# Performance work log

Measured on AMD Instinct MI355X. Metric: run time of the kernel, lower is better.

The kernel has to match this reference:

```python
import jax, jax.numpy as jnp
import numpy as np

NEG_SLOPE = 0.2
EPS = 1e-16  # PyG softmax denominator epsilon


def add_self_loops(edge_index, num_nodes):
    loop = jnp.arange(num_nodes, dtype=edge_index.dtype)
    src = jnp.concatenate([edge_index[0], loop])
    dst = jnp.concatenate([edge_index[1], loop])
    return src, dst


def gat_conv(x, src, dst, W, att_src, att_dst, bias, num_nodes):
    H, C = att_src.shape
    h = (x @ W).reshape(num_nodes, H, C)            # [N,H,C]
    a_s = jnp.einsum('nhc,hc->nh', h, att_src)      # [N,H]
    a_d = jnp.einsum('nhc,hc->nh', h, att_dst)
    e = jax.nn.leaky_relu(a_s[src] + a_d[dst], NEG_SLOPE)  # [E,H]
    m = jax.ops.segment_max(e, dst, num_segments=num_nodes)
    e = jnp.exp(e - m[dst])
    s = jax.ops.segment_sum(e, dst, num_segments=num_nodes)
    alpha = e / (s[dst] + EPS)                      # [E,H]
    out = jax.ops.segment_sum(h[src] * alpha[:, :, None], dst,
                              num_segments=num_nodes)  # [N,H,C]
    return out.reshape(num_nodes, H * C) + bias


def setup_inputs() -> dict:
    key = jax.random.key(0)
    ks = jax.random.split(key, 10)
    N, E, F, Ch = 50000, 800000, 128, 64
    sc = lambda f: 1.0 / np.sqrt(f)
    return {
        'x': jax.random.normal(ks[0], (N, F), jnp.float32),
        'edge_index': jax.random.randint(ks[1], (2, E), 0, N, jnp.int64),
        'W1': jax.random.normal(ks[2], (F, 4 * Ch), jnp.float32) * sc(F),
        'att_src1': jax.random.normal(ks[3], (4, Ch), jnp.float32) * sc(Ch),
        'att_dst1': jax.random.normal(ks[4], (4, Ch), jnp.float32) * sc(Ch),
        'b1': jnp.zeros((4 * Ch,), jnp.float32),
        'W2': jax.random.normal(ks[5], (4 * Ch, Ch), jnp.float32) * sc(4 * Ch),
        'att_src2': jax.random.normal(ks[6], (1, Ch), jnp.float32) * sc(Ch),
        'att_dst2': jax.random.normal(ks[7], (1, Ch), jnp.float32) * sc(Ch),
        'b2': jnp.zeros((Ch,), jnp.float32),
    }


def reference(x, edge_index, W1, att_src1, att_dst1, b1, W2, att_src2, att_dst2, b2):
    N = x.shape[0]
    src, dst = add_self_loops(edge_index, N)
    # dropout layers are inference no-ops
    h = gat_conv(x, src, dst, W1, att_src1, att_dst1, b1, N)
    h = jax.nn.elu(h)
    out = gat_conv(h, src, dst, W2, att_src2, att_dst2, b2, N)
    return out
```

## Files before the change

### kernel.cpp

```cpp
#include <hip/hip_runtime.h>
#include <hip/hip_bf16.h>
#include <stdint.h>


typedef __attribute__((ext_vector_type(8))) short bf16x8;
typedef __attribute__((ext_vector_type(4))) float f32x4;

__device__ __forceinline__ float bf2f(__hip_bfloat16 v) { return __bfloat162float(v); }
__device__ __forceinline__ float bfbits2f(unsigned short s) {
  union { uint32_t u; float f; } v; v.u = ((uint32_t)s) << 16; return v.f;
}
__device__ __forceinline__ unsigned short f2bfbits(float f) {
  union { float f; uint32_t u; } v; v.f = f;
  uint32_t u = v.u;
  return (unsigned short)((u + 0x7fffu + ((u >> 16) & 1u)) >> 16);
}

template <bool BF>
__device__ __forceinline__ float loadF(const void* p, size_t i) {
  if (BF) return bf2f(((const __hip_bfloat16*)p)[i]);
  return ((const float*)p)[i];
}
template <bool I64>
__device__ __forceinline__ int loadI(const void* p, size_t i) {
  if (I64) return (int)((const long long*)p)[i];
  return ((const int*)p)[i];
}
__device__ __forceinline__ float lrelu(float v) { return fmaxf(v, 0.2f * v); }

__global__ __launch_bounds__(256) void detect_zero(
    const uint32_t* __restrict__ xbits, const uint32_t* __restrict__ eibits,
    int* __restrict__ flags, int* __restrict__ zero_region, int nzero) {
  if (blockIdx.x == 0) {
    if (threadIdx.x < 64) {
      const int l = threadIdx.x;
      uint32_t u = xbits[l];
      uint32_t e = (u >> 23) & 0xffu;
      bool plausible = (e < 160u && e > 90u) || (u & 0x7fffffffu) == 0u;
      unsigned long long m1 = __ballot(plausible);
      bool z = (eibits[2 * l + 1] == 0u);
      unsigned long long m2 = __ballot(z);
      if (l == 0) {
        flags[0] = (__popcll(m1) < 32) ? 1 : 0;
        flags[1] = (m2 == ~0ULL) ? 1 : 0;
      }
    }
    return;
  }
  int i = (blockIdx.x - 1) * 256 + threadIdx.x;
  if (i < nzero) zero_region[i] = 0;
}

__global__ __launch_bounds__(256) void prep_all(
    const void* __restrict__ x, unsigned short* __restrict__ xb, size_t nx,
    const void* __restrict__ W1, unsigned short* __restrict__ w1t, int K1, int N1,
    const void* __restrict__ W2, unsigned short* __restrict__ w2t, int K2, int N2,
    int nb_cast, int nb_t1, const int* __restrict__ flags) {
  const int b = blockIdx.x;
  const bool f = flags[0] != 0;
  if (b < nb_cast) {
    size_t i = ((size_t)b * 256 + threadIdx.x) * 4;
    if (i >= nx) return;
    ushort4 o;
    if (f) {
      o = *(const ushort4*)((const unsigned short*)x + i);
    } else {
      float4 v = *(const float4*)((const float*)x + i);
      o.x = f2bfbits(v.x); o.y = f2bfbits(v.y);
      o.z = f2bfbits(v.z); o.w = f2bfbits(v.w);
    }
    *(ushort4*)(xb + i) = o;
  } else if (b < nb_cast + nb_t1) {
    int idx = (b - nb_cast) * 256 + threadIdx.x;
    if (idx >= K1 * N1) return;
    int k = idx / N1, n = idx - k * N1;
    float v = f ? loadF<true>(W1, idx) : loadF<false>(W1, idx);
    w1t[(size_t)n * K1 + k] = f2bfbits(v);
  } else {
    int idx = (b - nb_cast - nb_t1) * 256 + threadIdx.x;
    if (idx >= K2 * N2) return;
    int k = idx / N2, n = idx - k * N2;
    float v = f ? loadF<true>(W2, idx) : loadF<false>(W2, idx);
    w2t[(size_t)n * K2 + k] = f2bfbits(v);
  }
}

template <int KC, int NT, int HB>
__global__ __launch_bounds__(256, 4) void gemm_mfma_att(
    const unsigned short* __restrict__ A,
    const unsigned short* __restrict__ BT,
    unsigned short* __restrict__ C,
    const void* __restrict__ att_s, const void* __restrict__ att_d,
    float* __restrict__ as_o, float* __restrict__ ad_o,
    float* __restrict__ wself_o,
    int M, int Htot, const int* __restrict__ flags) {
  const int lane = threadIdx.x & 63;
  const int col = lane & 15;
  const int quad = lane >> 4;
  const int m0 = blockIdx.x * 64 + (threadIdx.x >> 6) * 16;
  const int n0 = blockIdx.y * (NT * 16);
  const int NCOL = Htot * 64;

  int gm = m0 + col;
  if (gm > M - 1) gm = M - 1;
  const unsigned short* arow = A + (size_t)gm * KC + quad * 8;
  const unsigned short* bbase = BT + (size_t)(n0 + col) * KC + quad * 8;

  f32x4 acc[NT] = {};
#pragma unroll
  for (int k0 = 0; k0 < KC; k0 += 32) {
    bf16x8 a = *(const bf16x8*)(arow + k0);
#pragma unroll
    for (int s = 0; s < NT; s++) {
      bf16x8 b = *(const bf16x8*)(bbase + (size_t)s * 16 * KC + k0);
      acc[s] = __builtin_amdgcn_mfma_f32_16x16x32_bf16(a, b, acc[s], 0, 0, 0);
    }
  }
#pragma unroll
  for (int s = 0; s < NT; s++)
#pragma unroll
    for (int r = 0; r < 4; r++) {
      int m = m0 + quad * 4 + r;
      if (m < M) C[(size_t)m * NCOL + n0 + s * 16 + col] = f2bfbits(acc[s][r]);
    }
  const int SC = NT / HB;
  const bool f = flags[0] != 0;
#pragma unroll
  for (int h = 0; h < HB; h++) {
    const int gh = blockIdx.y * HB + h;
    float ps[4] = {0.f, 0.f, 0.f, 0.f};
    float pd[4] = {0.f, 0.f, 0.f, 0.f};
#pragma unroll
    for (int j = 0; j < SC; j++) {
      int s = h * SC + j;
      int ci = gh * 64 + j * 16 + col;
      float av = f ? loadF<true>(att_s, ci) : loadF<false>(att_s, ci);
      float dv = f ? loadF<true>(att_d, ci) : loadF<false>(att_d, ci);
#pragma unroll
      for (int r = 0; r < 4; r++) {
        ps[r] += acc[s][r] * av;
        pd[r] += acc[s][r] * dv;
      }
    }
#pragma unroll
    for (int o = 1; o < 16; o <<= 1) {
#pragma unroll
      for (int r = 0; r < 4; r++) {
        ps[r] += __shfl_xor(ps[r], o);
        pd[r] += __shfl_xor(pd[r], o);
      }
    }
    if (col == 0) {
#pragma unroll
      for (int r = 0; r < 4; r++) {
        int m = m0 + quad * 4 + r;
        if (m < M) {
          as_o[m * Htot + gh] = ps[r];
          ad_o[m * Htot + gh] = pd[r];
          wself_o[m * Htot + gh] = __expf(lrelu(ps[r] + pd[r]));
        }
      }
    }
  }
}

__global__ void hist_kernel(const void* __restrict__ ei, int E,
                            int* __restrict__ deg, const int* __restrict__ flags) {
  int e = blockIdx.x * blockDim.x + threadIdx.x;
  if (e >= E) return;
  int d = flags[1] ? loadI<true>(ei, (size_t)E + e) : loadI<false>(ei, (size_t)E + e);
  atomicAdd(&deg[d], 1);
}

__global__ __launch_bounds__(256) void scan_block_sums(const int* __restrict__ deg,
                                                       int* __restrict__ bsum, int n) {
  __shared__ int buf[256];
  const int t = threadIdx.x;
  const int i = blockIdx.x * 256 + t;
  buf[t] = (i < n) ? deg[i] : 0;
  __syncthreads();
  for (int o = 128; o > 0; o >>= 1) {
    if (t < o) buf[t] += buf[t + o];
    __syncthreads();
  }
  if (t == 0) bsum[blockIdx.x] = buf[0];
}

__global__ __launch_bounds__(256) void scan_bsums(int* __restrict__ bsum, int nb) {
  __shared__ int buf[256];
  const int t = threadIdx.x;
  int orig = (t < nb) ? bsum[t] : 0;
  buf[t] = orig;
  __syncthreads();
  for (int o = 1; o < 256; o <<= 1) {
    int v = (t >= o) ? buf[t - o] : 0;
    __syncthreads();
    buf[t] += v;
    __syncthreads();
  }
  if (t < nb) bsum[t] = buf[t] - orig;
}

__global__ __launch_bounds__(256) void scan_finalize(const int* __restrict__ deg,
                                                     const int* __restrict__ bsum,
                                                     int* __restrict__ row_start, int n) {
  __shared__ int buf[256];
  const int t = threadIdx.x;
  const int i = blockIdx.x * 256 + t;
  int v = (i < n) ? deg[i] : 0;
  buf[t] = v;
  __syncthreads();
  for (int o = 1; o < 256; o <<= 1) {
    int x = (t >= o) ? buf[t - o] : 0;
    __syncthreads();
    buf[t] += x;
    __syncthreads();
  }
  if (i < n) row_start[i + 1] = bsum[blockIdx.x] + buf[t];
  if (i == 0) row_start[0] = 0;
}

__global__ void scatter_edges(const void* __restrict__ ei, int E,
                              const int* __restrict__ row_start,
                              int* __restrict__ cursor, int* __restrict__ col_src,
                              const int* __restrict__ flags) {
  int e = blockIdx.x * blockDim.x + threadIdx.x;
  if (e >= E) return;
  int s, d;
  if (flags[1]) { s = loadI<true>(ei, e);  d = loadI<true>(ei, (size_t)E + e); }
  else          { s = loadI<false>(ei, e); d = loadI<false>(ei, (size_t)E + e); }
  int pos = atomicAdd(&cursor[d], 1);
  col_src[row_start[d] + pos] = s;
}

__global__ __launch_bounds__(256) void aggregate4(
    const unsigned short* __restrict__ h_in,
    const float* __restrict__ wselfA,
    const float* __restrict__ as_,
    const float* __restrict__ ad_,
    const int* __restrict__ row_start, const int* __restrict__ col_src,
    const void* __restrict__ bias,
    unsigned short* __restrict__ out,
    int N, const int* __restrict__ flags) {
  const int dst = blockIdx.x * 4 + (threadIdx.x >> 6);
  if (dst >= N) return;
  const int l = threadIdx.x & 63;
  const int h = l >> 4;
  const int rs = row_start[dst];
  const int dg = row_start[dst + 1] - rs;
  const float ws = wselfA[dst * 4 + h];
  const float adv = ad_[dst * 4 + h];

  float a0, a1, a2, a3;
  {
    ushort4 sv = *(const ushort4*)(h_in + (size_t)dst * 256 + 4 * l);
    a0 = ws * bfbits2f(sv.x);
    a1 = ws * bfbits2f(sv.y);
    a2 = ws * bfbits2f(sv.z);
    a3 = ws * bfbits2f(sv.w);
  }
  float p = 0.f;
#pragma unroll 4
  for (int i = 0; i < dg; i++) {
    int sn = col_src[rs + i];
    float w = __expf(lrelu(as_[(size_t)sn * 4 + h] + adv));
    p += w;
    ushort4 sv = *(const ushort4*)(h_in + (size_t)sn * 256 + 4 * l);
    a0 += w * bfbits2f(sv.x);
    a1 += w * bfbits2f(sv.y);
    a2 += w * bfbits2f(sv.z);
    a3 += w * bfbits2f(sv.w);
  }
  const float inv = 1.0f / (p + ws + 1e-16f);
  const bool f = flags[0] != 0;
  float b0, b1, b2, b3;
  if (f) {
    b0 = loadF<true>(bias, 4 * l + 0); b1 = loadF<true>(bias, 4 * l + 1);
    b2 = loadF<true>(bias, 4 * l + 2); b3 = loadF<true>(bias, 4 * l + 3);
  } else {
    b0 = loadF<false>(bias, 4 * l + 0); b1 = loadF<false>(bias, 4 * l + 1);
    b2 = loadF<false>(bias, 4 * l + 2); b3 = loadF<false>(bias, 4 * l + 3);
  }
  float o0 = a0 * inv + b0, o1 = a1 * inv + b1;
  float o2 = a2 * inv + b2, o3 = a3 * inv + b3;
  o0 = o0 > 0.f ? o0 : __expf(o0) - 1.f;
  o1 = o1 > 0.f ? o1 : __expf(o1) - 1.f;
  o2 = o2 > 0.f ? o2 : __expf(o2) - 1.f;
  o3 = o3 > 0.f ? o3 : __expf(o3) - 1.f;
  ushort4 ov;
  ov.x = f2bfbits(o0); ov.y = f2bfbits(o1); ov.z = f2bfbits(o2); ov.w = f2bfbits(o3);
  *(ushort4*)(out + (size_t)dst * 256 + 4 * l) = ov;
}

__global__ __launch_bounds__(256) void aggregate1(
    const unsigned short* __restrict__ h_in,
    const float* __restrict__ wselfA,
    const float* __restrict__ as_,
    const float* __restrict__ ad_,
    const int* __restrict__ row_start, const int* __restrict__ col_src,
    const void* __restrict__ bias,
    void* __restrict__ out, int N, const int* __restrict__ flags) {
  const int dst = blockIdx.x * 4 + (threadIdx.x >> 6);
  if (dst >= N) return;
  const int l = threadIdx.x & 63;
  const int el = l & 15;
  const int slot = l >> 4;
  const int rs = row_start[dst];
  const int dg = row_start[dst + 1] - rs;
  const float ws = wselfA[dst];
  const float adv = ad_[dst];

  float a0 = 0.f, a1 = 0.f, a2 = 0.f, a3 = 0.f, p = 0.f;
  if (slot == 0) {
    ushort4 sv = *(const ushort4*)(h_in + (size_t)dst * 64 + 4 * el);
    a0 = ws * bfbits2f(sv.x);
    a1 = ws * bfbits2f(sv.y);
    a2 = ws * bfbits2f(sv.z);
    a3 = ws * bfbits2f(sv.w);
  }
#pragma unroll 2
  for (int i = slot; i < dg; i += 4) {
    int sn = col_src[rs + i];
    float w = __expf(lrelu(as_[sn] + adv));
    p += w;
    ushort4 sv = *(const ushort4*)(h_in + (size_t)sn * 64 + 4 * el);
    a0 += w * bfbits2f(sv.x);
    a1 += w * bfbits2f(sv.y);
    a2 += w * bfbits2f(sv.z);
    a3 += w * bfbits2f(sv.w);
  }
  a0 += __shfl_xor(a0, 16); a0 += __shfl_xor(a0, 32);
  a1 += __shfl_xor(a1, 16); a1 += __shfl_xor(a1, 32);
  a2 += __shfl_xor(a2, 16); a2 += __shfl_xor(a2, 32);
  a3 += __shfl_xor(a3, 16); a3 += __shfl_xor(a3, 32);
  p  += __shfl_xor(p, 16);  p  += __shfl_xor(p, 32);

  if (slot == 0) {
    const float inv = 1.0f / (p + ws + 1e-16f);
    const bool f = flags[0] != 0;
    float b0, b1, b2, b3;
    if (f) {
      b0 = loadF<true>(bias, 4 * el + 0); b1 = loadF<true>(bias, 4 * el + 1);
      b2 = loadF<true>(bias, 4 * el + 2); b3 = loadF<true>(bias, 4 * el + 3);
    } else {
      b0 = loadF<false>(bias, 4 * el + 0); b1 = loadF<false>(bias, 4 * el + 1);
      b2 = loadF<false>(bias, 4 * el + 2); b3 = loadF<false>(bias, 4 * el + 3);
    }
    float o0 = a0 * inv + b0, o1 = a1 * inv + b1;
    float o2 = a2 * inv + b2, o3 = a3 * inv + b3;
    size_t ob = (size_t)dst * 64 + 4 * el;
    if (f) {
      ushort4 ov;
      ov.x = f2bfbits(o0); ov.y = f2bfbits(o1);
      ov.z = f2bfbits(o2); ov.w = f2bfbits(o3);
      *(ushort4*)((unsigned short*)out + ob) = ov;
    } else {
      float4 ov; ov.x = o0; ov.y = o1; ov.z = o2; ov.w = o3;
      *(float4*)((float*)out + ob) = ov;
    }
  }
}

extern "C" void kernel_launch(void* const* d_in, const int* in_sizes, int n_in,
                              void* d_out, int out_size, void* d_ws, size_t ws_size,
                              hipStream_t stream) {
  const void* x    = d_in[0];
  const void* ei   = d_in[1];
  const void* W1   = d_in[2];
  const void* as1w = d_in[3];
  const void* ad1w = d_in[4];
  const void* b1   = d_in[5];
  const void* W2   = d_in[6];
  const void* as2w = d_in[7];
  const void* ad2w = d_in[8];
  const void* b2   = d_in[9];

  const int N  = out_size / 64;
  const int F  = in_sizes[0] / N;
  const int E  = in_sizes[1] / 2;
  const int H1 = in_sizes[3] / 64;
  const int D1 = H1 * 64;
  const int D2 = 64;

  size_t off = 0;
  auto alloc = [&](size_t bytes) -> void* {
    void* p = (char*)d_ws + off;
    off += (bytes + 255) & ~(size_t)255;
    return p;
  };
  int* flags = (int*)alloc(2 * sizeof(int));
  __hip_bfloat16* h1 = (__hip_bfloat16*)alloc((size_t)N * D1 * 2);
  __hip_bfloat16* x2 = (__hip_bfloat16*)alloc((size_t)N * D1 * 2);
  __hip_bfloat16* h2 = h1;
  unsigned short* xb  = (unsigned short*)alloc((size_t)N * F * 2);
  unsigned short* w1t = (unsigned short*)alloc((size_t)D1 * F * 2);
  unsigned short* w2t = (unsigned short*)alloc((size_t)D2 * D1 * 2);
  float* as1 = (float*)alloc((size_t)N * H1 * 4);
  float* ad1 = (float*)alloc((size_t)N * H1 * 4);
  float* wself1 = (float*)alloc((size_t)N * H1 * 4);
  float* as2 = (float*)alloc((size_t)N * 4);
  float* ad2 = (float*)alloc((size_t)N * 4);
  float* wself2 = (float*)alloc((size_t)N * 4);
  int* zero_region = (int*)alloc((size_t)2 * N * 4);
  int* deg = zero_region;
  int* cursor = zero_region + N;
  int* row_start = (int*)alloc((size_t)(N + 1) * 4);
  int* col_src = (int*)alloc((size_t)E * 4);
  int* bsum = (int*)alloc((size_t)256 * 4);
  (void)ws_size; (void)n_in;

  const int nb = (N + 255) / 256;
  const int eb = (E + 255) / 256;
  const int db = (N + 3) / 4;
  const int gb = (N + 63) / 64;
  const int nzero = 2 * N;
  const int zb = (nzero + 255) / 256;

  detect_zero<<<1 + zb, 256, 0, stream>>>((const uint32_t*)x, (const uint32_t*)ei,
                                          flags, zero_region, nzero);
  hist_kernel<<<eb, 256, 0, stream>>>(ei, E, deg, flags);
  scan_block_sums<<<nb, 256, 0, stream>>>(deg, bsum, N);
  scan_bsums<<<1, 256, 0, stream>>>(bsum, nb);
  scan_finalize<<<nb, 256, 0, stream>>>(deg, bsum, row_start, N);
  scatter_edges<<<eb, 256, 0, stream>>>(ei, E, row_start, cursor, col_src, flags);

  const size_t nx = (size_t)N * F;
  const int nb_cast = (int)((nx / 4 + 255) / 256);
  const int nb_t1 = (F * D1 + 255) / 256;
  const int nb_t2 = (D1 * D2 + 255) / 256;
  prep_all<<<nb_cast + nb_t1 + nb_t2, 256, 0, stream>>>(
      x, xb, nx, W1, w1t, F, D1, W2, w2t, D1, D2, nb_cast, nb_t1, flags);

  gemm_mfma_att<128, 8, 2><<<dim3(gb, 2), 256, 0, stream>>>(
      xb, w1t, (unsigned short*)h1, as1w, ad1w, as1, ad1, wself1, N, H1, flags);
  aggregate4<<<db, 256, 0, stream>>>((const unsigned short*)h1, wself1, as1, ad1,
                                     row_start, col_src, b1,
                                     (unsigned short*)x2, N, flags);

  gemm_mfma_att<256, 4, 1><<<dim3(gb, 1), 256, 0, stream>>>(
      (const unsigned short*)x2, w2t, (unsigned short*)h2, as2w, ad2w,
      as2, ad2, wself2, N, 1, flags);
  aggregate1<<<db, 256, 0, stream>>>((const unsigned short*)h2, wself2, as2, ad2,
                                     row_start, col_src, b2, d_out, N, flags);
}
```

Measured before the change: 331.3 us.

## Merge CSR build into fewer launches: fuse hist with prep, one-pass scan, scatter with GEMM1

```diff
diff --git a/kernel.cpp b/kernel.cpp
--- a/kernel.cpp
+++ b/kernel.cpp
@@ -51,33 +51,36 @@
   if (i < nzero) zero_region[i] = 0;
 }
 
-__global__ __launch_bounds__(256) void prep_all(
+__global__ __launch_bounds__(256) void hist_prep(
+    const void* __restrict__ ei, int E, int* __restrict__ deg,
     const void* __restrict__ x, unsigned short* __restrict__ xb, size_t nx,
     const void* __restrict__ W1, unsigned short* __restrict__ w1t, int K1, int N1,
     const void* __restrict__ W2, unsigned short* __restrict__ w2t, int K2, int N2,
-    int nb_cast, int nb_t1, const int* __restrict__ flags) {
+    int eb, int nb_cast, int nb_t1, const int* __restrict__ flags) {
   const int b = blockIdx.x;
   const bool f = flags[0] != 0;
-  if (b < nb_cast) {
-    size_t i = ((size_t)b * 256 + threadIdx.x) * 4;
+  if (b < eb) {
+    int e = b * 256 + threadIdx.x;
+    if (e >= E) return;
+    int d = flags[1] ? loadI<true>(ei, (size_t)E + e) : loadI<false>(ei, (size_t)E + e);
+    atomicAdd(&deg[d], 1);
+  } else if (b < eb + nb_cast) {
+    if (f) return;
+    size_t i = ((size_t)(b - eb) * 256 + threadIdx.x) * 4;
     if (i >= nx) return;
+    float4 v = *(const float4*)((const float*)x + i);
     ushort4 o;
-    if (f) {
-      o = *(const ushort4*)((const unsigned short*)x + i);
-    } else {
-      float4 v = *(const float4*)((const float*)x + i);
-      o.x = f2bfbits(v.x); o.y = f2bfbits(v.y);
-      o.z = f2bfbits(v.z); o.w = f2bfbits(v.w);
-    }
+    o.x = f2bfbits(v.x); o.y = f2bfbits(v.y);
+    o.z = f2bfbits(v.z); o.w = f2bfbits(v.w);
     *(ushort4*)(xb + i) = o;
-  } else if (b < nb_cast + nb_t1) {
-    int idx = (b - nb_cast) * 256 + threadIdx.x;
+  } else if (b < eb + nb_cast + nb_t1) {
+    int idx = (b - eb - nb_cast) * 256 + threadIdx.x;
     if (idx >= K1 * N1) return;
     int k = idx / N1, n = idx - k * N1;
     float v = f ? loadF<true>(W1, idx) : loadF<false>(W1, idx);
     w1t[(size_t)n * K1 + k] = f2bfbits(v);
   } else {
-    int idx = (b - nb_cast - nb_t1) * 256 + threadIdx.x;
+    int idx = (b - eb - nb_cast - nb_t1) * 256 + threadIdx.x;
     if (idx >= K2 * N2) return;
     int k = idx / N2, n = idx - k * N2;
     float v = f ? loadF<true>(W2, idx) : loadF<false>(W2, idx);
@@ -85,126 +88,11 @@
   }
 }
 
-template <int KC, int NT, int HB>
-__global__ __launch_bounds__(256, 4) void gemm_mfma_att(
-    const unsigned short* __restrict__ A,
-    const unsigned short* __restrict__ BT,
-    unsigned short* __restrict__ C,
-    const void* __restrict__ att_s, const void* __restrict__ att_d,
-    float* __restrict__ as_o, float* __restrict__ ad_o,
-    float* __restrict__ wself_o,
-    int M, int Htot, const int* __restrict__ flags) {
-  const int lane = threadIdx.x & 63;
-  const int col = lane & 15;
-  const int quad = lane >> 4;
-  const int m0 = blockIdx.x * 64 + (threadIdx.x >> 6) * 16;
-  const int n0 = blockIdx.y * (NT * 16);
-  const int NCOL = Htot * 64;
-
-  int gm = m0 + col;
-  if (gm > M - 1) gm = M - 1;
-  const unsigned short* arow = A + (size_t)gm * KC + quad * 8;
-  const unsigned short* bbase = BT + (size_t)(n0 + col) * KC + quad * 8;
-
-  f32x4 acc[NT] = {};
-#pragma unroll
-  for (int k0 = 0; k0 < KC; k0 += 32) {
-    bf16x8 a = *(const bf16x8*)(arow + k0);
-#pragma unroll
-    for (int s = 0; s < NT; s++) {
-      bf16x8 b = *(const bf16x8*)(bbase + (size_t)s * 16 * KC + k0);
-      acc[s] = __builtin_amdgcn_mfma_f32_16x16x32_bf16(a, b, acc[s], 0, 0, 0);
-    }
-  }
-#pragma unroll
-  for (int s = 0; s < NT; s++)
-#pragma unroll
-    for (int r = 0; r < 4; r++) {
-      int m = m0 + quad * 4 + r;
-      if (m < M) C[(size_t)m * NCOL + n0 + s * 16 + col] = f2bfbits(acc[s][r]);
-    }
-  const int SC = NT / HB;
-  const bool f = flags[0] != 0;
-#pragma unroll
-  for (int h = 0; h < HB; h++) {
-    const int gh = blockIdx.y * HB + h;
-    float ps[4] = {0.f, 0.f, 0.f, 0.f};
-    float pd[4] = {0.f, 0.f, 0.f, 0.f};
-#pragma unroll
-    for (int j = 0; j < SC; j++) {
-      int s = h * SC + j;
-      int ci = gh * 64 + j * 16 + col;
-      float av = f ? loadF<true>(att_s, ci) : loadF<false>(att_s, ci);
-      float dv = f ? loadF<true>(att_d, ci) : loadF<false>(att_d, ci);
-#pragma unroll
-      for (int r = 0; r < 4; r++) {
-        ps[r] += acc[s][r] * av;
-        pd[r] += acc[s][r] * dv;
-      }
-    }
-#pragma unroll
-    for (int o = 1; o < 16; o <<= 1) {
-#pragma unroll
-      for (int r = 0; r < 4; r++) {
-        ps[r] += __shfl_xor(ps[r], o);
-        pd[r] += __shfl_xor(pd[r], o);
-      }
-    }
-    if (col == 0) {
-#pragma unroll
-      for (int r = 0; r < 4; r++) {
-        int m = m0 + quad * 4 + r;
-        if (m < M) {
-          as_o[m * Htot + gh] = ps[r];
-          ad_o[m * Htot + gh] = pd[r];
-          wself_o[m * Htot + gh] = __expf(lrelu(ps[r] + pd[r]));
-        }
-      }
-    }
-  }
-}
-
-__global__ void hist_kernel(const void* __restrict__ ei, int E,
-                            int* __restrict__ deg, const int* __restrict__ flags) {
-  int e = blockIdx.x * blockDim.x + threadIdx.x;
-  if (e >= E) return;
-  int d = flags[1] ? loadI<true>(ei, (size_t)E + e) : loadI<false>(ei, (size_t)E + e);
-  atomicAdd(&deg[d], 1);
-}
-
-__global__ __launch_bounds__(256) void scan_block_sums(const int* __restrict__ deg,
-                                                       int* __restrict__ bsum, int n) {
+__global__ __launch_bounds__(256) void scan_onepass(
+    const int* __restrict__ deg, int* __restrict__ row_start,
+    int* __restrict__ total, int n) {
   __shared__ int buf[256];
-  const int t = threadIdx.x;
-  const int i = blockIdx.x * 256 + t;
-  buf[t] = (i < n) ? deg[i] : 0;
-  __syncthreads();
-  for (int o = 128; o > 0; o >>= 1) {
-    if (t < o) buf[t] += buf[t + o];
-    __syncthreads();
-  }
-  if (t == 0) bsum[blockIdx.x] = buf[0];
-}
-
-__global__ __launch_bounds__(256) void scan_bsums(int* __restrict__ bsum, int nb) {
-  __shared__ int buf[256];
-  const int t = threadIdx.x;
-  int orig = (t < nb) ? bsum[t] : 0;
-  buf[t] = orig;
-  __syncthreads();
-  for (int o = 1; o < 256; o <<= 1) {
-    int v = (t >= o) ? buf[t - o] : 0;
-    __syncthreads();
-    buf[t] += v;
-    __syncthreads();
-  }
-  if (t < nb) bsum[t] = buf[t] - orig;
-}
-
-__global__ __launch_bounds__(256) void scan_finalize(const int* __restrict__ deg,
-                                                     const int* __restrict__ bsum,
-                                                     int* __restrict__ row_start, int n) {
-  __shared__ int buf[256];
+  __shared__ int sbase;
   const int t = threadIdx.x;
   const int i = blockIdx.x * 256 + t;
   int v = (i < n) ? deg[i] : 0;
@@ -216,21 +104,131 @@
     buf[t] += x;
     __syncthreads();
   }
-  if (i < n) row_start[i + 1] = bsum[blockIdx.x] + buf[t];
-  if (i == 0) row_start[0] = 0;
-}
-
-__global__ void scatter_edges(const void* __restrict__ ei, int E,
-                              const int* __restrict__ row_start,
-                              int* __restrict__ cursor, int* __restrict__ col_src,
-                              const int* __restrict__ flags) {
-  int e = blockIdx.x * blockDim.x + threadIdx.x;
-  if (e >= E) return;
-  int s, d;
-  if (flags[1]) { s = loadI<true>(ei, e);  d = loadI<true>(ei, (size_t)E + e); }
-  else          { s = loadI<false>(ei, e); d = loadI<false>(ei, (size_t)E + e); }
-  int pos = atomicAdd(&cursor[d], 1);
-  col_src[row_start[d] + pos] = s;
+  if (t == 255) sbase = atomicAdd(total, buf[255]);
+  __syncthreads();
+  if (i < n) row_start[i] = sbase + buf[t] - v;
+}
+
+template <int KC, int NT, int HB>
+__device__ __forceinline__ void gemm_body(
+    int bx, int by, int tid,
+    const unsigned short* __restrict__ A,
+    const unsigned short* __restrict__ BT,
+    unsigned short* __restrict__ C,
+    const void* __restrict__ att_s, const void* __restrict__ att_d,
+    float* __restrict__ as_o, float* __restrict__ ad_o,
+    float* __restrict__ wself_o,
+    int M, int Htot, bool f) {
+  const int lane = tid & 63;
+  const int col = lane & 15;
+  const int quad = lane >> 4;
+  const int m0 = bx * 64 + (tid >> 6) * 16;
+  const int n0 = by * (NT * 16);
+  const int NCOL = Htot * 64;
+
+  int gm = m0 + col;
+  if (gm > M - 1) gm = M - 1;
+  const unsigned short* arow = A + (size_t)gm * KC + quad * 8;
+  const unsigned short* bbase = BT + (size_t)(n0 + col) * KC + quad * 8;
+
+  f32x4 acc[NT] = {};
+#pragma unroll
+  for (int k0 = 0; k0 < KC; k0 += 32) {
+    bf16x8 a = *(const bf16x8*)(arow + k0);
+#pragma unroll
+    for (int s = 0; s < NT; s++) {
+      bf16x8 b = *(const bf16x8*)(bbase + (size_t)s * 16 * KC + k0);
+      acc[s] = __builtin_amdgcn_mfma_f32_16x16x32_bf16(a, b, acc[s], 0, 0, 0);
+    }
+  }
+#pragma unroll
+  for (int s = 0; s < NT; s++)
+#pragma unroll
+    for (int r = 0; r < 4; r++) {
+      int m = m0 + quad * 4 + r;
+      if (m < M) C[(size_t)m * NCOL + n0 + s * 16 + col] = f2bfbits(acc[s][r]);
+    }
+  const int SC = NT / HB;
+#pragma unroll
+  for (int h = 0; h < HB; h++) {
+    const int gh = by * HB + h;
+    float ps[4] = {0.f, 0.f, 0.f, 0.f};
+    float pd[4] = {0.f, 0.f, 0.f, 0.f};
+#pragma unroll
+    for (int j = 0; j < SC; j++) {
+      int s = h * SC + j;
+      int ci = gh * 64 + j * 16 + col;
+      float av = f ? loadF<true>(att_s, ci) : loadF<false>(att_s, ci);
+      float dv = f ? loadF<true>(att_d, ci) : loadF<false>(att_d, ci);
+#pragma unroll
+      for (int r = 0; r < 4; r++) {
+        ps[r] += acc[s][r] * av;
+        pd[r] += acc[s][r] * dv;
+      }
+    }
+#pragma unroll
+    for (int o = 1; o < 16; o <<= 1) {
+#pragma unroll
+      for (int r = 0; r < 4; r++) {
+        ps[r] += __shfl_xor(ps[r], o);
+        pd[r] += __shfl_xor(pd[r], o);
+      }
+    }
+    if (col == 0) {
+#pragma unroll
+      for (int r = 0; r < 4; r++) {
+        int m = m0 + quad * 4 + r;
+        if (m < M) {
+          as_o[m * Htot + gh] = ps[r];
+          ad_o[m * Htot + gh] = pd[r];
+          wself_o[m * Htot + gh] = __expf(lrelu(ps[r] + pd[r]));
+        }
+      }
+    }
+  }
+}
+
+__global__ __launch_bounds__(256, 4) void scatter_gemm1(
+    const void* __restrict__ ei, int E, const int* __restrict__ row_start,
+    int* __restrict__ cursor, int* __restrict__ col_src,
+    int eb, int gb,
+    const unsigned short* __restrict__ xb, const void* __restrict__ x,
+    const unsigned short* __restrict__ w1t,
+    unsigned short* __restrict__ C,
+    const void* __restrict__ att_s, const void* __restrict__ att_d,
+    float* __restrict__ as_o, float* __restrict__ ad_o,
+    float* __restrict__ wself_o,
+    int M, int Htot, const int* __restrict__ flags) {
+  const int b = blockIdx.x;
+  if (b < eb) {
+    int e = b * 256 + threadIdx.x;
+    if (e >= E) return;
+    int s, d;
+    if (flags[1]) { s = loadI<true>(ei, e);  d = loadI<true>(ei, (size_t)E + e); }
+    else          { s = loadI<false>(ei, e); d = loadI<false>(ei, (size_t)E + e); }
+    int pos = atomicAdd(&cursor[d], 1);
+    col_src[row_start[d] + pos] = s;
+  } else {
+    const int bb = b - eb;
+    const int bx = bb % gb, by = bb / gb;
+    const bool f = flags[0] != 0;
+    const unsigned short* Ap = f ? (const unsigned short*)x : xb;
+    gemm_body<128, 8, 2>(bx, by, threadIdx.x, Ap, w1t, C, att_s, att_d,
+                         as_o, ad_o, wself_o, M, Htot, f);
+  }
+}
+
+template <int KC, int NT, int HB>
+__global__ __launch_bounds__(256, 4) void gemm_kernel(
+    const unsigned short* __restrict__ A, const unsigned short* __restrict__ BT,
+    unsigned short* __restrict__ C,
+    const void* __restrict__ att_s, const void* __restrict__ att_d,
+    float* __restrict__ as_o, float* __restrict__ ad_o,
+    float* __restrict__ wself_o,
+    int M, int Htot, const int* __restrict__ flags) {
+  gemm_body<KC, NT, HB>(blockIdx.x, blockIdx.y, threadIdx.x, A, BT, C,
+                        att_s, att_d, as_o, ad_o, wself_o, M, Htot,
+                        flags[0] != 0);
 }
 
 __global__ __launch_bounds__(256) void aggregate4(
@@ -238,7 +236,8 @@
     const float* __restrict__ wselfA,
     const float* __restrict__ as_,
     const float* __restrict__ ad_,
-    const int* __restrict__ row_start, const int* __restrict__ col_src,
+    const int* __restrict__ row_start, const int* __restrict__ deg,
+    const int* __restrict__ col_src,
     const void* __restrict__ bias,
     unsigned short* __restrict__ out,
     int N, const int* __restrict__ flags) {
@@ -247,7 +246,7 @@
   const int l = threadIdx.x & 63;
   const int h = l >> 4;
   const int rs = row_start[dst];
-  const int dg = row_start[dst + 1] - rs;
+  const int dg = deg[dst];
   const float ws = wselfA[dst * 4 + h];
   const float adv = ad_[dst * 4 + h];
 
@@ -297,7 +296,8 @@
     const float* __restrict__ wselfA,
     const float* __restrict__ as_,
     const float* __restrict__ ad_,
-    const int* __restrict__ row_start, const int* __restrict__ col_src,
+    const int* __restrict__ row_start, const int* __restrict__ deg,
+    const int* __restrict__ col_src,
     const void* __restrict__ bias,
     void* __restrict__ out, int N, const int* __restrict__ flags) {
   const int dst = blockIdx.x * 4 + (threadIdx.x >> 6);
@@ -306,7 +306,7 @@
   const int el = l & 15;
   const int slot = l >> 4;
   const int rs = row_start[dst];
-  const int dg = row_start[dst + 1] - rs;
+  const int dg = deg[dst];
   const float ws = wselfA[dst];
   const float adv = ad_[dst];
 
@@ -401,45 +401,41 @@
   float* as2 = (float*)alloc((size_t)N * 4);
   float* ad2 = (float*)alloc((size_t)N * 4);
   float* wself2 = (float*)alloc((size_t)N * 4);
-  int* zero_region = (int*)alloc((size_t)2 * N * 4);
+  int* zero_region = (int*)alloc((size_t)(2 * N + 64) * 4);
   int* deg = zero_region;
   int* cursor = zero_region + N;
+  int* total = zero_region + 2 * N;
   int* row_start = (int*)alloc((size_t)(N + 1) * 4);
   int* col_src = (int*)alloc((size_t)E * 4);
-  int* bsum = (int*)alloc((size_t)256 * 4);
   (void)ws_size; (void)n_in;
 
   const int nb = (N + 255) / 256;
   const int eb = (E + 255) / 256;
   const int db = (N + 3) / 4;
   const int gb = (N + 63) / 64;
-  const int nzero = 2 * N;
+  const int nzero = 2 * N + 64;
   const int zb = (nzero + 255) / 256;
-
-  detect_zero<<<1 + zb, 256, 0, stream>>>((const uint32_t*)x, (const uint32_t*)ei,
-                                          flags, zero_region, nzero);
-  hist_kernel<<<eb, 256, 0, stream>>>(ei, E, deg, flags);
-  scan_block_sums<<<nb, 256, 0, stream>>>(deg, bsum, N);
-  scan_bsums<<<1, 256, 0, stream>>>(bsum, nb);
-  scan_finalize<<<nb, 256, 0, stream>>>(deg, bsum, row_start, N);
-  scatter_edges<<<eb, 256, 0, stream>>>(ei, E, row_start, cursor, col_src, flags);
 
   const size_t nx = (size_t)N * F;
   const int nb_cast = (int)((nx / 4 + 255) / 256);
   const int nb_t1 = (F * D1 + 255) / 256;
   const int nb_t2 = (D1 * D2 + 255) / 256;
-  prep_all<<<nb_cast + nb_t1 + nb_t2, 256, 0, stream>>>(
-      x, xb, nx, W1, w1t, F, D1, W2, w2t, D1, D2, nb_cast, nb_t1, flags);
-
-  gemm_mfma_att<128, 8, 2><<<dim3(gb, 2), 256, 0, stream>>>(
-      xb, w1t, (unsigned short*)h1, as1w, ad1w, as1, ad1, wself1, N, H1, flags);
+
+  detect_zero<<<1 + zb, 256, 0, stream>>>((const uint32_t*)x, (const uint32_t*)ei,
+                                          flags, zero_region, nzero);
+  hist_prep<<<eb + nb_cast + nb_t1 + nb_t2, 256, 0, stream>>>(
+      ei, E, deg, x, xb, nx, W1, w1t, F, D1, W2, w2t, D1, D2,
+      eb, nb_cast, nb_t1, flags);
+  scan_onepass<<<nb, 256, 0, stream>>>(deg, row_start, total, N);
+  scatter_gemm1<<<eb + gb * 2, 256, 0, stream>>>(
+      ei, E, row_start, cursor, col_src, eb, gb,
+      xb, x, w1t, (unsigned short*)h1, as1w, ad1w, as1, ad1, wself1, N, H1, flags);
   aggregate4<<<db, 256, 0, stream>>>((const unsigned short*)h1, wself1, as1, ad1,
-                                     row_start, col_src, b1,
+                                     row_start, deg, col_src, b1,
                                      (unsigned short*)x2, N, flags);
-
-  gemm_mfma_att<256, 4, 1><<<dim3(gb, 1), 256, 0, stream>>>(
+  gemm_kernel<256, 4, 1><<<dim3(gb, 1), 256, 0, stream>>>(
       (const unsigned short*)x2, w2t, (unsigned short*)h2, as2w, ad2w,
       as2, ad2, wself2, N, 1, flags);
   aggregate1<<<db, 256, 0, stream>>>((const unsigned short*)h2, wself2, as2, ad2,
-                                     row_start, col_src, b2, d_out, N, flags);
-}
+                                     row_start, deg, col_src, b2, d_out, N, flags);
+}
```

New measurement: 319.9 us. 3.4% less time.
